# Performance work log

Hardware: AMD Instinct MI355X
Metric: run time of the kernel (lower is better)

The kernel has to match this reference:

```python
import jax, jax.numpy as jnp
import numpy as np

B, T, C, FFN, N_LAYER, LAYER_ID = 4, 2048, 1024, 4096, 24, 1
EPS = 1e-5


def setup_inputs() -> dict:
    key = jax.random.key(0)
    ks = jax.random.split(key, 10)
    scale = 0.02

    def w(k, shape):
        return (jax.random.normal(k, shape, jnp.float32) * scale)

    # RWKV-4 init formulas for layer_id=1, n_layer=24 (learned params, init per source)
    r01 = LAYER_ID / (N_LAYER - 1)
    r10 = 1.0 - LAYER_ID / N_LAYER
    ddd = np.arange(C, dtype=np.float64) / C
    h = np.arange(C, dtype=np.float64)
    decay = -5.0 + 8.0 * (h / (C - 1)) ** (0.7 + 1.3 * r01)
    zigzag = np.array([(i + 1) % 3 - 1 for i in range(C)], dtype=np.float64) * 0.5
    tfirst = np.log(0.3) + zigzag

    return {
        "x": jax.random.normal(ks[0], (B, T, C), jnp.float32),
        "ln1_w": jnp.ones((C,), jnp.float32), "ln1_b": jnp.zeros((C,), jnp.float32),
        "ln2_w": jnp.ones((C,), jnp.float32), "ln2_b": jnp.zeros((C,), jnp.float32),
        "time_decay": jnp.asarray(decay, jnp.float32),
        "time_first": jnp.asarray(tfirst, jnp.float32),
        "tmk": jnp.asarray(ddd ** r10, jnp.float32),
        "tmv": jnp.asarray(ddd ** r10 + 0.3 * r01, jnp.float32),
        "tmr": jnp.asarray(ddd ** (0.5 * r10), jnp.float32),
        "att_kw": w(ks[1], (C, C)), "att_vw": w(ks[2], (C, C)),
        "att_rw": w(ks[3], (C, C)), "att_ow": w(ks[4], (C, C)),
        "f_tmk": jnp.asarray(ddd ** r10, jnp.float32),
        "f_tmr": jnp.asarray(ddd ** r10, jnp.float32),
        "f_kw": w(ks[5], (FFN, C)), "f_rw": w(ks[6], (C, C)), "f_vw": w(ks[7], (C, FFN)),
    }


def _ln(z, g, b):
    m = jnp.mean(z, axis=-1, keepdims=True)
    v = jnp.mean(jnp.square(z - m), axis=-1, keepdims=True)
    return (z - m) * jax.lax.rsqrt(v + EPS) * g + b


def _shift(z):  # token shift: prepend zero row along T, drop last
    return jnp.pad(z, ((0, 0), (1, 0), (0, 0)))[:, :-1]


def _wkv(time_decay, u, k, v):
    # Numerically-stable RWKV-4 WKV recurrence (log-space max trick).
    # k, v: [B, T, C]; time_decay, u: [C]
    w = -jnp.exp(time_decay)  # per-channel decay (negative)
    kt = jnp.moveaxis(k, 1, 0)  # [T, B, C]
    vt = jnp.moveaxis(v, 1, 0)
    aa = jnp.zeros_like(kt[0])
    bb = jnp.zeros_like(kt[0])
    pp = jnp.full_like(kt[0], -1e38)

    def step(carry, kv):
        aa, bb, pp = carry
        kk, vv = kv
        ww = u + kk
        p = jnp.maximum(pp, ww)
        e1 = jnp.exp(pp - p)
        e2 = jnp.exp(ww - p)
        out = (e1 * aa + e2 * vv) / (e1 * bb + e2)
        ww2 = pp + w
        p2 = jnp.maximum(ww2, kk)
        e1b = jnp.exp(ww2 - p2)
        e2b = jnp.exp(kk - p2)
        return (e1b * aa + e2b * vv, e1b * bb + e2b, p2), out

    _, out = jax.lax.scan(step, (aa, bb, pp), (kt, vt))
    return jnp.moveaxis(out, 0, 1)  # [B, T, C]


def reference(x, ln1_w, ln1_b, ln2_w, ln2_b, time_decay, time_first,
              tmk, tmv, tmr, att_kw, att_vw, att_rw, att_ow,
              f_tmk, f_tmr, f_kw, f_rw, f_vw):
    # --- RWKV_TimeMix (layer_id != 0; protectors are identity in fwd for finite vals) ---
    h = _ln(x, ln1_w, ln1_b)
    hx = _shift(h)
    xk = h * tmk + hx * (1.0 - tmk)
    xv = h * tmv + hx * (1.0 - tmv)
    xr = h * tmr + hx * (1.0 - tmr)
    k = jnp.einsum('btc,dc->btd', xk, att_kw)
    v = jnp.einsum('btc,dc->btd', xv, att_vw)
    sr = jax.nn.sigmoid(jnp.einsum('btc,dc->btd', xr, att_rw))
    rwkv = sr * _wkv(time_decay, time_first, k, v)
    x = x + jnp.einsum('btd,cd->btc', rwkv, att_ow)
    # --- RWKV_ChannelMix ---
    h = _ln(x, ln2_w, ln2_b)
    hx = _shift(h)
    xk = h * f_tmk + hx * (1.0 - f_tmk)
    xr = h * f_tmr + hx * (1.0 - f_tmr)
    kk = jnp.square(jax.nn.relu(jnp.einsum('btc,fc->btf', xk, f_kw)))
    kv = jnp.einsum('btf,cf->btc', kk, f_vw)
    x = x + jax.nn.sigmoid(jnp.einsum('btc,dc->btd', xr, f_rw)) * kv
    return x
```

## Files before the change

### kernel.cpp

```cpp
#include <hip/hip_runtime.h>
#include <cstdint>

#define C_DIM 1024
#define T_DIM 2048
#define B_DIM 4
#define FFN_DIM 4096
#define NROWS (B_DIM * T_DIM)
#define NELEM ((size_t)NROWS * C_DIM)
#define MB ((size_t)1 << 20)
#define NSEG 32
#define SEGL (T_DIM / NSEG)

typedef __bf16 bf16;
typedef __bf16 bf16x4 __attribute__((ext_vector_type(4)));
typedef __bf16 bf16x8 __attribute__((ext_vector_type(8)));
typedef float  floatx4 __attribute__((ext_vector_type(4)));

#define GLDS(g, l) __builtin_amdgcn_global_load_lds(                          \
    (const __attribute__((address_space(1))) void*)(g),                       \
    (__attribute__((address_space(3))) void*)(l), 16, 0, 0)

struct W7 {
    const float* s[7];
    bf16*        d[7];
    int          cum[8];
};

__global__ __launch_bounds__(256) void f2b7_kernel(W7 w)
{
    int id = blockIdx.x * 256 + threadIdx.x;
    int seg = 0;
#pragma unroll
    for (int j = 1; j < 7; ++j) if (id >= w.cum[j]) seg = j;
    int i = id - w.cum[seg];
    float4 v = ((const float4*)w.s[seg])[i];
    bf16x4 o = { (bf16)v.x, (bf16)v.y, (bf16)v.z, (bf16)v.w };
    ((bf16x4*)w.d[seg])[i] = o;
}

template<bool HASV>
__global__ __launch_bounds__(256) void lnmix_kernel(const float* __restrict__ x,
                                                    const float* __restrict__ g,
                                                    const float* __restrict__ b,
                                                    const float* __restrict__ mk,
                                                    const float* __restrict__ mv,
                                                    const float* __restrict__ mr,
                                                    bf16* __restrict__ xk,
                                                    bf16* __restrict__ xv,
                                                    bf16* __restrict__ xr)
{
    int row = blockIdx.x;
    int t   = row & (T_DIM - 1);
    int tid = threadIdx.x;
    size_t i4 = (size_t)row * 256 + tid;

    float4 v  = ((const float4*)x)[i4];
    float4 vp = make_float4(0.f, 0.f, 0.f, 0.f);
    if (t != 0) vp = ((const float4*)x)[i4 - 256];

    float s   = v.x + v.y + v.z + v.w;
    float s2  = v.x * v.x + v.y * v.y + v.z * v.z + v.w * v.w;
    float sp  = vp.x + vp.y + vp.z + vp.w;
    float sp2 = vp.x * vp.x + vp.y * vp.y + vp.z * vp.z + vp.w * vp.w;
    for (int off = 32; off > 0; off >>= 1) {
        s   += __shfl_down(s,   off);
        s2  += __shfl_down(s2,  off);
        sp  += __shfl_down(sp,  off);
        sp2 += __shfl_down(sp2, off);
    }
    __shared__ float red[16];
    int lane = tid & 63, wid = tid >> 6;
    if (lane == 0) { red[wid] = s; red[4 + wid] = s2; red[8 + wid] = sp; red[12 + wid] = sp2; }
    __syncthreads();
    s   = red[0] + red[1] + red[2] + red[3];
    s2  = red[4] + red[5] + red[6] + red[7];
    sp  = red[8] + red[9] + red[10] + red[11];
    sp2 = red[12] + red[13] + red[14] + red[15];

    float mean  = s * (1.0f / C_DIM);
    float inv   = rsqrtf(s2 * (1.0f / C_DIM) - mean * mean + 1e-5f);
    float meanp = sp * (1.0f / C_DIM);
    float invp  = rsqrtf(sp2 * (1.0f / C_DIM) - meanp * meanp + 1e-5f);

    float4 gv = ((const float4*)g)[tid];
    float4 bv = ((const float4*)b)[tid];
    float4 hv, hp;
    hv.x = (v.x - mean) * inv * gv.x + bv.x;
    hv.y = (v.y - mean) * inv * gv.y + bv.y;
    hv.z = (v.z - mean) * inv * gv.z + bv.z;
    hv.w = (v.w - mean) * inv * gv.w + bv.w;
    if (t != 0) {
        hp.x = (vp.x - meanp) * invp * gv.x + bv.x;
        hp.y = (vp.y - meanp) * invp * gv.y + bv.y;
        hp.z = (vp.z - meanp) * invp * gv.z + bv.z;
        hp.w = (vp.w - meanp) * invp * gv.w + bv.w;
    } else {
        hp = make_float4(0.f, 0.f, 0.f, 0.f);
    }

    float4 m1 = ((const float4*)mk)[tid];
    bf16x4 o;
    o.x = (bf16)(hp.x + m1.x * (hv.x - hp.x));
    o.y = (bf16)(hp.y + m1.y * (hv.y - hp.y));
    o.z = (bf16)(hp.z + m1.z * (hv.z - hp.z));
    o.w = (bf16)(hp.w + m1.w * (hv.w - hp.w));
    ((bf16x4*)xk)[i4] = o;

    if (HASV) {
        float4 m2 = ((const float4*)mv)[tid];
        o.x = (bf16)(hp.x + m2.x * (hv.x - hp.x));
        o.y = (bf16)(hp.y + m2.y * (hv.y - hp.y));
        o.z = (bf16)(hp.z + m2.z * (hv.z - hp.z));
        o.w = (bf16)(hp.w + m2.w * (hv.w - hp.w));
        ((bf16x4*)xv)[i4] = o;
    }

    float4 m3 = ((const float4*)mr)[tid];
    o.x = (bf16)(hp.x + m3.x * (hv.x - hp.x));
    o.y = (bf16)(hp.y + m3.y * (hv.y - hp.y));
    o.z = (bf16)(hp.z + m3.z * (hv.z - hp.z));
    o.w = (bf16)(hp.w + m3.w * (hv.w - hp.w));
    ((bf16x4*)xr)[i4] = o;
}

#define EPI_NONE 0
#define EPI_SIG 1
#define EPI_RELU2 2
#define EPI_ADD 3
#define EPI_SCALEADD 4

struct GemmProb {
    const bf16* A;
    const bf16* W;
    void*       Y;
    const float* X2;
    const bf16*  S;
    int N, K, epi, outBf16;
};
struct GemmBatch {
    GemmProb p[3];
    int cum[4];
};

template<int BN>
__global__ __launch_bounds__(256) void gemm_bat(GemmBatch bat)
{
    constexpr int NJ = BN / 32;
    __shared__ unsigned short As[128 * 32];
    __shared__ unsigned short Bs[BN * 32];

    int tid = threadIdx.x;
    int id  = blockIdx.x;
    int pi  = (id >= bat.cum[1]) + (id >= bat.cum[2]);
    const bf16* PA = bat.p[pi].A;
    const bf16* PW = bat.p[pi].W;
    void*       PY = bat.p[pi].Y;
    const float* PX2 = bat.p[pi].X2;
    const bf16*  PS  = bat.p[pi].S;
    int N = bat.p[pi].N, K = bat.p[pi].K;
    int epi = bat.p[pi].epi, obf = bat.p[pi].outBf16;
    int lid = id - bat.cum[pi];

    int ntn    = N / BN;
    int stride = ntn >> 3;
    int sh     = __ffs(stride) - 1;
    int sq  = lid >> 3;
    int n_t = (lid & 7) * stride + (sq & (stride - 1));
    int m_t = sq >> sh;
    int m0 = m_t * 128, n0 = n_t * BN;

    int r0  = tid >> 2;
    int qsw = ((tid & 3) - ((r0 >> 1) & 3)) & 3;
    const bf16* Ag = PA + (size_t)(m0 + r0) * K + qsw * 8;
    const bf16* Wg = PW + (size_t)(n0 + r0) * K + qsw * 8;
    size_t rowK = (size_t)64 * K;
    int wv = tid >> 6;
    unsigned short* AsW0 = As + wv * 512;
    unsigned short* AsW1 = As + 2048 + wv * 512;
    unsigned short* BsW0 = Bs + wv * 512;
    unsigned short* BsW1 = Bs + (BN == 128 ? 2048 : 0) + wv * 512;

    int ln = tid & 63;
    int wm = (wv & 1) * 64, wn = (wv >> 1) * (BN / 2);
    int ra0 = wm + (ln & 15);
    int rb0 = wn + (ln & 15);
    int qa  = ln >> 4;
    int abase = ra0 * 32 + (((qa + (ra0 >> 1)) & 3) * 8);
    int bbase = rb0 * 32 + (((qa + (rb0 >> 1)) & 3) * 8);

    floatx4 acc[4][NJ] = {};

    for (int k0 = 0; k0 < K; k0 += 32) {
        if (k0) __syncthreads();
        GLDS(Ag + k0,        AsW0);
        GLDS(Ag + k0 + rowK, AsW1);
        GLDS(Wg + k0,        BsW0);
        if constexpr (BN == 128) GLDS(Wg + k0 + rowK, BsW1);
        __syncthreads();

        bf16x8 a[4], b[NJ];
#pragma unroll
        for (int i = 0; i < 4; ++i) a[i] = *(const bf16x8*)(As + abase + i * 512);
#pragma unroll
        for (int j = 0; j < NJ; ++j) b[j] = *(const bf16x8*)(Bs + bbase + j * 512);
#pragma unroll
        for (int i = 0; i < 4; ++i)
#pragma unroll
            for (int j = 0; j < NJ; ++j)
                acc[i][j] = __builtin_amdgcn_mfma_f32_16x16x32_bf16(a[i], b[j], acc[i][j], 0, 0, 0);
    }

    int row0 = (ln >> 4) * 4;
    int colb = n0 + wn + (ln & 15);
#pragma unroll
    for (int i = 0; i < 4; ++i) {
        int gm = m0 + wm + i * 16 + row0;
#pragma unroll
        for (int j = 0; j < NJ; ++j) {
            int gn = colb + j * 16;
#pragma unroll
            for (int r = 0; r < 4; ++r) {
                size_t idx = (size_t)(gm + r) * N + gn;
                float v = acc[i][j][r];
                if (epi == EPI_SIG)        v = 1.0f / (1.0f + __expf(-v));
                else if (epi == EPI_RELU2) { float t2 = fmaxf(v, 0.0f); v = t2 * t2; }
                else if (epi == EPI_ADD)   v = PX2[idx] + v;
                else if (epi == EPI_SCALEADD) v = PX2[idx] + (float)PS[idx] * v;
                if (obf) ((bf16*)PY)[idx] = (bf16)v;
                else     ((float*)PY)[idx] = v;
            }
        }
    }
}

__global__ __launch_bounds__(256) void wkv_seg(const float* __restrict__ k,
                                               const float* __restrict__ v,
                                               const float* __restrict__ decay,
                                               float* __restrict__ sa,
                                               float* __restrict__ sb,
                                               float* __restrict__ sp)
{
    int idx = blockIdx.x * 256 + threadIdx.x;
    int c   = idx & (C_DIM - 1);
    int bs  = idx >> 10;
    int seg = bs & (NSEG - 1);
    int b   = bs >> 5;
    float w = -__expf(decay[c]);
    size_t base = ((size_t)b * T_DIM + (size_t)seg * SEGL) * C_DIM + c;
    float aa = 0.f, bb = 0.f, pp = -1e38f;
    for (int t = 0; t < SEGL; ++t) {
        size_t off = base + (size_t)t * C_DIM;
        float kk = k[off], vv = v[off];
        float ww2 = pp + w;
        float p2  = fmaxf(ww2, kk);
        float e1  = __expf(ww2 - p2);
        float e2  = __expf(kk - p2);
        aa = e1 * aa + e2 * vv;
        bb = e1 * bb + e2;
        pp = p2;
    }
    sa[idx] = aa; sb[idx] = bb; sp[idx] = pp;
}

__global__ __launch_bounds__(256) void wkv_comb(const float* __restrict__ sa,
                                                const float* __restrict__ sb,
                                                const float* __restrict__ sp,
                                                const float* __restrict__ decay,
                                                float* __restrict__ ia,
                                                float* __restrict__ ib,
                                                float* __restrict__ ip)
{
    int idx = blockIdx.x * 256 + threadIdx.x;
    int c = idx & (C_DIM - 1);
    int b = idx >> 10;
    float wL = -__expf(decay[c]) * (float)SEGL;
    float aa = 0.f, bb = 0.f, pp = -1e38f;
    size_t base = (size_t)b * NSEG * C_DIM + c;
    for (int j = 0; j < NSEG; ++j) {
        size_t o = base + (size_t)j * C_DIM;
        ia[o] = aa; ib[o] = bb; ip[o] = pp;
        float a_s = sa[o], b_s = sb[o], p_s = sp[o];
        float pd = pp + wL;
        float pn = fmaxf(pd, p_s);
        float e1 = __expf(pd - pn);
        float e2 = __expf(p_s - pn);
        aa = e1 * aa + e2 * a_s;
        bb = e1 * bb + e2 * b_s;
        pp = pn;
    }
}

__global__ __launch_bounds__(256) void wkv_out(const float* __restrict__ k,
                                               const float* __restrict__ v,
                                               const bf16* __restrict__ sr,
                                               const float* __restrict__ decay,
                                               const float* __restrict__ first,
                                               const float* __restrict__ ia,
                                               const float* __restrict__ ib,
                                               const float* __restrict__ ip,
                                               bf16* __restrict__ out)
{
    int idx = blockIdx.x * 256 + threadIdx.x;
    int c   = idx & (C_DIM - 1);
    int bs  = idx >> 10;
    int seg = bs & (NSEG - 1);
    int b   = bs >> 5;
    float w = -__expf(decay[c]);
    float u = first[c];
    float aa = ia[idx], bb = ib[idx], pp = ip[idx];
    size_t base = ((size_t)b * T_DIM + (size_t)seg * SEGL) * C_DIM + c;
    for (int t = 0; t < SEGL; ++t) {
        size_t off = base + (size_t)t * C_DIM;
        float kk = k[off], vv = v[off];
        float ww = u + kk;
        float p  = fmaxf(pp, ww);
        float e1 = __expf(pp - p);
        float e2 = __expf(ww - p);
        float o  = (e1 * aa + e2 * vv) / (e1 * bb + e2);
        out[off] = (bf16)((float)sr[off] * o);
        float ww2 = pp + w;
        float p2  = fmaxf(ww2, kk);
        float e1b = __expf(ww2 - p2);
        float e2b = __expf(kk - p2);
        aa = e1b * aa + e2b * vv;
        bb = e1b * bb + e2b;
        pp = p2;
    }
}

extern "C" void kernel_launch(void* const* d_in, const int* in_sizes, int n_in,
                              void* d_out, int out_size, void* d_ws, size_t ws_size,
                              hipStream_t stream)
{
    const float* x          = (const float*)d_in[0];
    const float* ln1_w      = (const float*)d_in[1];
    const float* ln1_b      = (const float*)d_in[2];
    const float* ln2_w      = (const float*)d_in[3];
    const float* ln2_b      = (const float*)d_in[4];
    const float* time_decay = (const float*)d_in[5];
    const float* time_first = (const float*)d_in[6];
    const float* tmk        = (const float*)d_in[7];
    const float* tmv        = (const float*)d_in[8];
    const float* tmr        = (const float*)d_in[9];
    const float* att_kw     = (const float*)d_in[10];
    const float* att_vw     = (const float*)d_in[11];
    const float* att_rw     = (const float*)d_in[12];
    const float* att_ow     = (const float*)d_in[13];
    const float* f_tmk      = (const float*)d_in[14];
    const float* f_tmr      = (const float*)d_in[15];
    const float* f_kw       = (const float*)d_in[16];
    const float* f_rw       = (const float*)d_in[17];
    const float* f_vw       = (const float*)d_in[18];
    float* out = (float*)d_out;

    char* W8 = (char*)d_ws;
    bf16* kw_b  = (bf16*)(W8 + 0 * MB);
    bf16* vw_b  = (bf16*)(W8 + 2 * MB);
    bf16* rw_b  = (bf16*)(W8 + 4 * MB);
    bf16* ow_b  = (bf16*)(W8 + 6 * MB);
    bf16* fkw_b = (bf16*)(W8 + 8 * MB);
    bf16* frw_b = (bf16*)(W8 + 16 * MB);
    bf16* fvw_b = (bf16*)(W8 + 18 * MB);

    bf16*  xk_b   = (bf16*)(W8 + 26 * MB);
    bf16*  xv_b   = (bf16*)(W8 + 42 * MB);
    bf16*  xr_b   = (bf16*)(W8 + 58 * MB);
    bf16*  rwkv_b = xk_b;
    bf16*  xk2_b  = (bf16*)(W8 + 26 * MB);
    bf16*  xr2_b  = (bf16*)(W8 + 42 * MB);
    bf16*  sr2_b  = (bf16*)(W8 + 58 * MB);
    float* kbuf   = (float*)(W8 + 74 * MB);
    float* vbuf   = (float*)(W8 + 106 * MB);
    bf16*  srb_b  = (bf16*)(W8 + 138 * MB);
    bf16*  kk_b   = (bf16*)(W8 + 106 * MB);

    size_t KB512 = (size_t)512 * 1024;
    float* sc_a = (float*)(W8 + 170 * MB);
    float* sc_b = (float*)(W8 + 170 * MB + 1 * KB512);
    float* sc_p = (float*)(W8 + 170 * MB + 2 * KB512);
    float* in_a = (float*)(W8 + 170 * MB + 3 * KB512);
    float* in_b = (float*)(W8 + 170 * MB + 4 * KB512);
    float* in_p = (float*)(W8 + 170 * MB + 5 * KB512);

    int nC4 = C_DIM * C_DIM / 4, nF4 = FFN_DIM * C_DIM / 4;
    W7 w7;
    const float* srcs[7] = { att_kw, att_vw, att_rw, att_ow, f_kw, f_rw, f_vw };
    bf16*        dsts[7] = { kw_b, vw_b, rw_b, ow_b, fkw_b, frw_b, fvw_b };
    int          cnts[7] = { nC4, nC4, nC4, nC4, nF4, nC4, nF4 };
    int cum = 0;
    for (int i = 0; i < 7; ++i) { w7.s[i] = srcs[i]; w7.d[i] = dsts[i]; w7.cum[i] = cum; cum += cnts[i]; }
    w7.cum[7] = cum;
    f2b7_kernel<<<cum / 256, 256, 0, stream>>>(w7);

    int segGrid = B_DIM * NSEG * C_DIM / 256;

    auto prob = [](const bf16* A, const bf16* W, void* Y, const float* X2,
                   const bf16* S, int N, int K, int epi, int obf) {
        GemmProb p; p.A = A; p.W = W; p.Y = Y; p.X2 = X2; p.S = S;
        p.N = N; p.K = K; p.epi = epi; p.outBf16 = obf; return p;
    };

    lnmix_kernel<true><<<NROWS, 256, 0, stream>>>(x, ln1_w, ln1_b, tmk, tmv, tmr,
                                                  xk_b, xv_b, xr_b);
    {
        GemmBatch b3;
        b3.p[0] = prob(xk_b, kw_b, kbuf,  nullptr, nullptr, C_DIM, C_DIM, EPI_NONE, 0);
        b3.p[1] = prob(xv_b, vw_b, vbuf,  nullptr, nullptr, C_DIM, C_DIM, EPI_NONE, 0);
        b3.p[2] = prob(xr_b, rw_b, srb_b, nullptr, nullptr, C_DIM, C_DIM, EPI_SIG,  1);
        b3.cum[0] = 0; b3.cum[1] = 512; b3.cum[2] = 1024; b3.cum[3] = 1536;
        gemm_bat<128><<<1536, 256, 0, stream>>>(b3);
    }
    wkv_seg<<<segGrid, 256, 0, stream>>>(kbuf, vbuf, time_decay, sc_a, sc_b, sc_p);
    wkv_comb<<<B_DIM * C_DIM / 256, 256, 0, stream>>>(sc_a, sc_b, sc_p, time_decay, in_a, in_b, in_p);
    wkv_out<<<segGrid, 256, 0, stream>>>(kbuf, vbuf, srb_b, time_decay, time_first,
                                         in_a, in_b, in_p, rwkv_b);
    {
        GemmBatch b1;
        b1.p[0] = prob(rwkv_b, ow_b, out, x, nullptr, C_DIM, C_DIM, EPI_ADD, 0);
        b1.p[1] = b1.p[0]; b1.p[2] = b1.p[0];
        b1.cum[0] = 0; b1.cum[1] = 1024; b1.cum[2] = 1024; b1.cum[3] = 1024;
        gemm_bat<64><<<1024, 256, 0, stream>>>(b1);
    }

    lnmix_kernel<false><<<NROWS, 256, 0, stream>>>(out, ln2_w, ln2_b, f_tmk, nullptr, f_tmr,
                                                   xk2_b, nullptr, xr2_b);
    {
        GemmBatch b2;
        b2.p[0] = prob(xk2_b, fkw_b, kk_b,  nullptr, nullptr, FFN_DIM, C_DIM, EPI_RELU2, 1);
        b2.p[1] = prob(xr2_b, frw_b, sr2_b, nullptr, nullptr, C_DIM,   C_DIM, EPI_SIG,   1);
        b2.p[2] = b2.p[1];
        b2.cum[0] = 0; b2.cum[1] = 2048; b2.cum[2] = 2560; b2.cum[3] = 2560;
        gemm_bat<128><<<2560, 256, 0, stream>>>(b2);
    }
    {
        GemmBatch b1;
        b1.p[0] = prob(kk_b, fvw_b, out, out, sr2_b, C_DIM, FFN_DIM, EPI_SCALEADD, 0);
        b1.p[1] = b1.p[0]; b1.p[2] = b1.p[0];
        b1.cum[0] = 0; b1.cum[1] = 1024; b1.cum[2] = 1024; b1.cum[3] = 1024;
        gemm_bat<64><<<1024, 256, 0, stream>>>(b1);
    }
}
```

Before: 580.9 us.

## Double-buffer LDS tiles in batched GEMM to overlap global loads with MFMA

Doubles the shared-memory A/B tiles and prefetches the next K-slice via global_load_lds while the current slice feeds MFMAs, replacing the two per-iteration syncthreads with one waitcnt+barrier. MFMA issue priority is also raised with s_setprio. This is meant to hide global load latency in the GEMM main loop. In exchange it doubles LDS use per block, which may reduce occupancy, and the single barrier relies on the explicit vmcnt wait for correctness.

```diff
diff --git a/kernel.cpp b/kernel.cpp
--- a/kernel.cpp
+++ b/kernel.cpp
@@ -145,9 +145,11 @@
 template<int BN>
 __global__ __launch_bounds__(256) void gemm_bat(GemmBatch bat)
 {
-    constexpr int NJ = BN / 32;
-    __shared__ unsigned short As[128 * 32];
-    __shared__ unsigned short Bs[BN * 32];
+    constexpr int NJ   = BN / 32;
+    constexpr int ABUF = 128 * 32;
+    constexpr int BBUF = BN * 32;
+    __shared__ unsigned short As[2 * ABUF];
+    __shared__ unsigned short Bs[2 * BBUF];
 
     int tid = threadIdx.x;
     int id  = blockIdx.x;
@@ -190,24 +192,43 @@
 
     floatx4 acc[4][NJ] = {};
 
-    for (int k0 = 0; k0 < K; k0 += 32) {
-        if (k0) __syncthreads();
-        GLDS(Ag + k0,        AsW0);
-        GLDS(Ag + k0 + rowK, AsW1);
-        GLDS(Wg + k0,        BsW0);
-        if constexpr (BN == 128) GLDS(Wg + k0 + rowK, BsW1);
-        __syncthreads();
-
+    GLDS(Ag,        AsW0);
+    GLDS(Ag + rowK, AsW1);
+    GLDS(Wg,        BsW0);
+    if constexpr (BN == 128) GLDS(Wg + rowK, BsW1);
+    asm volatile("s_waitcnt vmcnt(0)" ::: "memory");
+    __builtin_amdgcn_s_barrier();
+
+    int nt  = K >> 5;
+    int cur = 0;
+    for (int t = 0; t < nt; ++t) {
+        if (t + 1 < nt) {
+            int koff = (t + 1) << 5;
+            int nb   = cur ^ 1;
+            GLDS(Ag + koff,        AsW0 + nb * ABUF);
+            GLDS(Ag + koff + rowK, AsW1 + nb * ABUF);
+            GLDS(Wg + koff,        BsW0 + nb * BBUF);
+            if constexpr (BN == 128) GLDS(Wg + koff + rowK, BsW1 + nb * BBUF);
+        }
+        const unsigned short* Ac = As + cur * ABUF + abase;
+        const unsigned short* Bc = Bs + cur * BBUF + bbase;
         bf16x8 a[4], b[NJ];
 #pragma unroll
-        for (int i = 0; i < 4; ++i) a[i] = *(const bf16x8*)(As + abase + i * 512);
-#pragma unroll
-        for (int j = 0; j < NJ; ++j) b[j] = *(const bf16x8*)(Bs + bbase + j * 512);
+        for (int i = 0; i < 4; ++i) a[i] = *(const bf16x8*)(Ac + i * 512);
+#pragma unroll
+        for (int j = 0; j < NJ; ++j) b[j] = *(const bf16x8*)(Bc + j * 512);
+        asm volatile("s_waitcnt lgkmcnt(0)" ::: "memory");
+        __builtin_amdgcn_sched_barrier(0);
+        __builtin_amdgcn_s_setprio(1);
 #pragma unroll
         for (int i = 0; i < 4; ++i)
 #pragma unroll
             for (int j = 0; j < NJ; ++j)
                 acc[i][j] = __builtin_amdgcn_mfma_f32_16x16x32_bf16(a[i], b[j], acc[i][j], 0, 0, 0);
+        __builtin_amdgcn_s_setprio(0);
+        asm volatile("s_waitcnt vmcnt(0)" ::: "memory");
+        __builtin_amdgcn_s_barrier();
+        cur ^= 1;
     }
 
     int row0 = (ln >> 4) * 4;
```

Result: no change. 585.3 us (+0.7%).
